# Kernel optimization log

Hardware: AMD Instinct MI355X
Metric: run time of the kernel (lower is better)

The kernel has to match this reference:

```python
import jax, jax.numpy as jnp
import numpy as np

B, S, H = 2, 2048, 2048
NH, NKV, D = 32, 8, 64
THETA = 10000.0
SCALE = 1.0 / float(np.sqrt(D))


def setup_inputs() -> dict:
    key = jax.random.key(0)
    k1, k2, k3 = jax.random.split(key, 3)
    return {
        "positions": jnp.arange(S, dtype=jnp.int32),
        "hidden_states": jax.random.normal(k1, (B, S, H), dtype=jnp.float32),
        "Wqkv": jax.random.normal(k2, (H, (NH + 2 * NKV) * D), dtype=jnp.float32) * 0.02,
        "Wo": jax.random.normal(k3, (NH * D, H), dtype=jnp.float32) * 0.02,
    }


def _rope_neox(x, cos, sin):
    # x: [B,S,h,D]; NeoX style: rotate_half over full rotary dim
    half = D // 2
    rot = jnp.concatenate([-x[..., half:], x[..., :half]], axis=-1)
    return x * cos + rot * sin


def reference(positions, hidden_states, Wqkv, Wo):
    # fused QKV projection
    qkv = jnp.einsum('bsh,hf->bsf', hidden_states, Wqkv)  # [B,S,(NH+2NKV)*D]
    q, k, v = jnp.split(qkv, [NH * D, NH * D + NKV * D], axis=-1)
    q = q.reshape(B, S, NH, D)
    k = k.reshape(B, S, NKV, D)
    v = v.reshape(B, S, NKV, D)

    # inline RoPE (full head_dim, NeoX style)
    inv_freq = 1.0 / (THETA ** (jnp.arange(0, D, 2, dtype=jnp.float32) / D))  # [D/2]
    freqs = positions.astype(jnp.float32)[:, None] * inv_freq  # [S,D/2]
    cos = jnp.concatenate([jnp.cos(freqs)] * 2, axis=-1)[None, :, None, :]  # [1,S,1,D]
    sin = jnp.concatenate([jnp.sin(freqs)] * 2, axis=-1)[None, :, None, :]
    q = _rope_neox(q, cos, sin)
    k = _rope_neox(k, cos, sin)

    # GQA: expand KV heads to match query heads
    g = NH // NKV
    k = jnp.repeat(k, g, axis=2)  # [B,S,NH,D]
    v = jnp.repeat(v, g, axis=2)

    # causal attention (prefill over the cached sequence)
    scores = jnp.einsum('bqhd,bkhd->bhqk', q, k) * SCALE  # [B,NH,S,S]
    causal = jnp.tril(jnp.ones((S, S), dtype=bool))
    scores = jnp.where(causal[None, None], scores, jnp.finfo(scores.dtype).min)
    attn = jax.nn.softmax(scores, axis=-1)
    ctx = jnp.einsum('bhqk,bkhd->bqhd', attn, v).reshape(B, S, NH * D)

    # output projection
    return jnp.einsum('bsf,fh->bsh', ctx, Wo)
```

## Files before the change

kernel.cpp:

```cpp
#include <hip/hip_runtime.h>
#include <hip/hip_bf16.h>
#include <math.h>

#define B_ 2
#define S_ 2048
#define H_ 2048
#define NH_ 32
#define NKV_ 8
#define D_ 64
#define F_ 3072
#define SCALE_ 0.125f
#define QSCALE_ 0.18033688011112042f
#define LN1E4_32_ 0.28782313662425575f

using bf16 = __bf16;
using bf16x4 = __attribute__((ext_vector_type(4))) __bf16;
using bf16x8 = __attribute__((ext_vector_type(8))) __bf16;
using f32x4 = __attribute__((ext_vector_type(4))) float;

#define GLOBAL_AS(p) ((__attribute__((address_space(1))) void*)(p))
#define LDS_AS(p)    ((__attribute__((address_space(3))) void*)(p))

__global__ void cvt_f32_bf16(const float4* __restrict__ in, bf16* __restrict__ out, int n4) {
    int i = blockIdx.x * 256 + threadIdx.x;
    if (i >= n4) return;
    float4 v = in[i];
    bf16x4 o = {(bf16)v.x, (bf16)v.y, (bf16)v.z, (bf16)v.w};
    *reinterpret_cast<bf16x4*>(out + (size_t)i * 4) = o;
}

__global__ void transpose_to_bf16(const float* __restrict__ in, bf16* __restrict__ out,
                                  int K, int N) {
    __shared__ float tile[32][33];
    int n0 = blockIdx.x * 32, k0 = blockIdx.y * 32;
    int tx = threadIdx.x, ty = threadIdx.y;
#pragma unroll
    for (int i = 0; i < 4; ++i)
        tile[ty + i * 8][tx] = in[(size_t)(k0 + ty + i * 8) * N + n0 + tx];
    __syncthreads();
#pragma unroll
    for (int i = 0; i < 4; ++i)
        out[(size_t)(n0 + ty + i * 8) * K + k0 + tx] = (bf16)tile[tx][ty + i * 8];
}

__global__ __launch_bounds__(256) void gemm_qkv_rope(const bf16* __restrict__ A,
                                                     const bf16* __restrict__ BT,
                                                     const int* __restrict__ positions,
                                                     bf16* __restrict__ Q,
                                                     bf16* __restrict__ Kb,
                                                     bf16* __restrict__ Vt) {
    __shared__ __attribute__((aligned(16))) bf16 As[128 * 32];
    __shared__ __attribute__((aligned(16))) bf16 Bs[128 * 32];
    const int tid = threadIdx.x;
    const int w = tid >> 6, lane = tid & 63;
    const int t = lane & 15, quad = lane >> 4;
    const int m0 = blockIdx.y * 128, n0 = blockIdx.x * 128;
    const int wm = (w >> 1) * 64, wn = (w & 1) * 64;
    const int lrow = lane >> 2;
    const int lcol = (lane & 3) * 8;

    f32x4 acc[4][4] = {};

    for (int k0 = 0; k0 < H_; k0 += 32) {
#pragma unroll
        for (int i = 0; i < 2; ++i) {
            int c = w * 2 + i;
            const bf16* ga = A + (size_t)(m0 + c * 16 + lrow) * H_ + k0 + lcol;
            __builtin_amdgcn_global_load_lds(GLOBAL_AS(ga), LDS_AS(As + c * 512), 16, 0, 0);
            const bf16* gb = BT + (size_t)(n0 + c * 16 + lrow) * H_ + k0 + lcol;
            __builtin_amdgcn_global_load_lds(GLOBAL_AS(gb), LDS_AS(Bs + c * 512), 16, 0, 0);
        }
        __syncthreads();
        bf16x8 a[4], b[4];
#pragma unroll
        for (int i = 0; i < 4; ++i)
            a[i] = *reinterpret_cast<const bf16x8*>(As + (wm + i * 16 + t) * 32 + quad * 8);
#pragma unroll
        for (int j = 0; j < 4; ++j)
            b[j] = *reinterpret_cast<const bf16x8*>(Bs + (wn + j * 16 + t) * 32 + quad * 8);
#pragma unroll
        for (int i = 0; i < 4; ++i)
#pragma unroll
            for (int j = 0; j < 4; ++j)
                acc[i][j] = __builtin_amdgcn_mfma_f32_16x16x32_bf16(a[i], b[j], acc[i][j], 0, 0, 0);
        __syncthreads();
    }

    const int hseg = (n0 + wn) >> 6;
    if (hseg < NH_ + NKV_) {
        const bool isQ = hseg < NH_;
        const float qs = isQ ? QSCALE_ : 1.0f;
        bf16* dst = isQ ? Q : Kb;
        const int hh = isQ ? hseg : hseg - NH_;
        const int nh = isQ ? NH_ : NKV_;
        const float inv0 = __expf(-(float)t * LN1E4_32_);
        const float inv1 = inv0 * 0.01f;
#pragma unroll
        for (int i = 0; i < 4; ++i)
#pragma unroll
            for (int r = 0; r < 4; ++r) {
                const int mrow = m0 + wm + i * 16 + quad * 4 + r;
                const int s = mrow & (S_ - 1), b = mrow >> 11;
                const float pos = (float)positions[s];
                float sn0, cs0, sn1, cs1;
                sincosf(pos * inv0, &sn0, &cs0);
                sincosf(pos * inv1, &sn1, &cs1);
                const float x0 = acc[i][0][r], x1 = acc[i][1][r];
                const float x2 = acc[i][2][r], x3 = acc[i][3][r];
                bf16 o0 = (bf16)((x0 * cs0 - x2 * sn0) * qs);
                bf16 o1 = (bf16)((x1 * cs1 - x3 * sn1) * qs);
                bf16 o2 = (bf16)((x2 * cs0 + x0 * sn0) * qs);
                bf16 o3 = (bf16)((x3 * cs1 + x1 * sn1) * qs);
                bf16* p = dst + ((size_t)(b * nh + hh) * S_ + s) * D_;
                p[t] = o0;
                p[16 + t] = o1;
                p[32 + t] = o2;
                p[48 + t] = o3;
            }
    } else {
        const int hv = hseg - NH_ - NKV_;
#pragma unroll
        for (int i = 0; i < 4; ++i)
#pragma unroll
            for (int r = 0; r < 4; ++r) {
                const int mrow = m0 + wm + i * 16 + quad * 4 + r;
                const int s = mrow & (S_ - 1), b = mrow >> 11;
                bf16* p = Vt + ((size_t)(b * NKV_ + hv) * D_) * S_ + s;
#pragma unroll
                for (int j = 0; j < 4; ++j)
                    p[(size_t)(j * 16 + t) * S_] = (bf16)acc[i][j][r];
            }
    }
}

__global__ __launch_bounds__(256) void gemm_bt(const bf16* __restrict__ A,
                                               const bf16* __restrict__ BT,
                                               float* __restrict__ C,
                                               int M, int N, int K) {
    __shared__ __attribute__((aligned(16))) bf16 As[128 * 32];
    __shared__ __attribute__((aligned(16))) bf16 Bs[128 * 32];
    const int tid = threadIdx.x;
    const int w = tid >> 6, lane = tid & 63;
    const int t = lane & 15, quad = lane >> 4;
    const int m0 = blockIdx.y * 128, n0 = blockIdx.x * 128;
    const int wm = (w >> 1) * 64, wn = (w & 1) * 64;
    const int lrow = lane >> 2;
    const int lcol = (lane & 3) * 8;

    f32x4 acc[4][4] = {};

    for (int k0 = 0; k0 < K; k0 += 32) {
#pragma unroll
        for (int i = 0; i < 2; ++i) {
            int c = w * 2 + i;
            const bf16* ga = A + (size_t)(m0 + c * 16 + lrow) * K + k0 + lcol;
            __builtin_amdgcn_global_load_lds(GLOBAL_AS(ga), LDS_AS(As + c * 512), 16, 0, 0);
            const bf16* gb = BT + (size_t)(n0 + c * 16 + lrow) * K + k0 + lcol;
            __builtin_amdgcn_global_load_lds(GLOBAL_AS(gb), LDS_AS(Bs + c * 512), 16, 0, 0);
        }
        __syncthreads();
        bf16x8 a[4], b[4];
#pragma unroll
        for (int i = 0; i < 4; ++i)
            a[i] = *reinterpret_cast<const bf16x8*>(As + (wm + i * 16 + t) * 32 + quad * 8);
#pragma unroll
        for (int j = 0; j < 4; ++j)
            b[j] = *reinterpret_cast<const bf16x8*>(Bs + (wn + j * 16 + t) * 32 + quad * 8);
#pragma unroll
        for (int i = 0; i < 4; ++i)
#pragma unroll
            for (int j = 0; j < 4; ++j)
                acc[i][j] = __builtin_amdgcn_mfma_f32_16x16x32_bf16(a[i], b[j], acc[i][j], 0, 0, 0);
        __syncthreads();
    }
#pragma unroll
    for (int i = 0; i < 4; ++i)
#pragma unroll
        for (int j = 0; j < 4; ++j)
#pragma unroll
            for (int r = 0; r < 4; ++r)
                C[(size_t)(m0 + wm + i * 16 + quad * 4 + r) * N + n0 + wn + j * 16 + t] =
                    acc[i][j][r];
}

__global__ __launch_bounds__(256, 4) void flash_attn(const bf16* __restrict__ Q,
                                                     const bf16* __restrict__ Kb,
                                                     const bf16* __restrict__ Vt,
                                                     bf16* __restrict__ ctx) {
    __shared__ __attribute__((aligned(16))) bf16 Ks[8 * 512];
    __shared__ __attribute__((aligned(16))) bf16 Vs[8 * 512];
    __shared__ __attribute__((aligned(16))) bf16 Plds[4][16 * 72];
    const int tid = threadIdx.x;
    const int w = tid >> 6, lane = tid & 63;
    const int t = lane & 15, quad = lane >> 4;
    const int kvh = blockIdx.y, b = blockIdx.z;
    const int h = kvh * 4 + w;
    const int bh = b * NH_ + h;
    const int bhk = b * NKV_ + kvh;
    const bf16* Kbase = Kb + (size_t)bhk * S_ * D_;
    const bf16* Vbase = Vt + (size_t)bhk * D_ * S_;

    for (int rep = 0; rep < 2; ++rep) {
        const int tileIdx = rep ? (127 - (int)blockIdx.x) : (int)blockIdx.x;
        const int qbase = tileIdx * 16;
        const int kend = qbase + 16;

        const bf16* Qp = Q + ((size_t)bh * S_ + qbase) * D_;
        bf16x8 qf0 = *reinterpret_cast<const bf16x8*>(Qp + t * D_ + quad * 8);
        bf16x8 qf1 = *reinterpret_cast<const bf16x8*>(Qp + t * D_ + 32 + quad * 8);

        f32x4 o[4] = {};
        float m = -1e30f, l = 0.f;

        for (int k0 = 0; k0 < kend; k0 += 64) {
            __syncthreads();
#pragma unroll
            for (int j = 0; j < 4; ++j) {
                const int c = w * 4 + j;
                if (c < 8) {
                    const int tl = c & 3, hf = c >> 2;
                    const bf16* src =
                        Kbase + (size_t)(k0 + tl * 16 + t) * D_ + hf * 32 + quad * 8;
                    __builtin_amdgcn_global_load_lds(GLOBAL_AS(src), LDS_AS(Ks + c * 512), 16, 0,
                                                     0);
                } else {
                    const int cv = c - 8, dt = cv & 3, hf = cv >> 2;
                    const bf16* src =
                        Vbase + (size_t)(dt * 16 + t) * S_ + k0 + hf * 32 + quad * 8;
                    __builtin_amdgcn_global_load_lds(GLOBAL_AS(src), LDS_AS(Vs + cv * 512), 16, 0,
                                                     0);
                }
            }
            __syncthreads();

            f32x4 sa[4] = {};
#pragma unroll
            for (int tl = 0; tl < 4; ++tl) {
                bf16x8 kf0 = *reinterpret_cast<const bf16x8*>(Ks + (tl)*512 + lane * 8);
                bf16x8 kf1 = *reinterpret_cast<const bf16x8*>(Ks + (4 + tl) * 512 + lane * 8);
                sa[tl] = __builtin_amdgcn_mfma_f32_16x16x32_bf16(kf0, qf0, sa[tl], 0, 0, 0);
                sa[tl] = __builtin_amdgcn_mfma_f32_16x16x32_bf16(kf1, qf1, sa[tl], 0, 0, 0);
            }
            if (k0 + 64 >= kend) {
                const int qrow = qbase + t;
#pragma unroll
                for (int tl = 0; tl < 4; ++tl)
#pragma unroll
                    for (int r = 0; r < 4; ++r)
                        if (k0 + tl * 16 + quad * 4 + r > qrow) sa[tl][r] = -1e30f;
            }
            float mx = -1e30f;
#pragma unroll
            for (int tl = 0; tl < 4; ++tl)
#pragma unroll
                for (int r = 0; r < 4; ++r) mx = fmaxf(mx, sa[tl][r]);
            mx = fmaxf(mx, __shfl_xor(mx, 16, 64));
            mx = fmaxf(mx, __shfl_xor(mx, 32, 64));
            const float mn = fmaxf(m, mx);
            const float alpha = exp2f(m - mn);
            m = mn;
            float rs = 0.f;
#pragma unroll
            for (int tl = 0; tl < 4; ++tl) {
                float p0 = exp2f(sa[tl][0] - mn);
                float p1 = exp2f(sa[tl][1] - mn);
                float p2 = exp2f(sa[tl][2] - mn);
                float p3 = exp2f(sa[tl][3] - mn);
                rs += (p0 + p1) + (p2 + p3);
                bf16x4 pk = {(bf16)p0, (bf16)p1, (bf16)p2, (bf16)p3};
                *reinterpret_cast<bf16x4*>(&Plds[w][t * 72 + tl * 16 + quad * 4]) = pk;
            }
#pragma unroll
            for (int dt = 0; dt < 4; ++dt)
#pragma unroll
                for (int r = 0; r < 4; ++r) o[dt][r] *= alpha;
            rs += __shfl_xor(rs, 16, 64);
            rs += __shfl_xor(rs, 32, 64);
            l = l * alpha + rs;

            asm volatile("s_waitcnt lgkmcnt(0)" ::: "memory");
            bf16x8 pf0 = *reinterpret_cast<const bf16x8*>(&Plds[w][t * 72 + quad * 8]);
            bf16x8 pf1 = *reinterpret_cast<const bf16x8*>(&Plds[w][t * 72 + 32 + quad * 8]);
            asm volatile("" ::: "memory");
#pragma unroll
            for (int dt = 0; dt < 4; ++dt) {
                bf16x8 vf0 = *reinterpret_cast<const bf16x8*>(Vs + (dt)*512 + lane * 8);
                bf16x8 vf1 = *reinterpret_cast<const bf16x8*>(Vs + (4 + dt) * 512 + lane * 8);
                o[dt] = __builtin_amdgcn_mfma_f32_16x16x32_bf16(vf0, pf0, o[dt], 0, 0, 0);
                o[dt] = __builtin_amdgcn_mfma_f32_16x16x32_bf16(vf1, pf1, o[dt], 0, 0, 0);
            }
        }
        const float inv = 1.0f / l;
        const size_t row = (size_t)b * S_ + qbase + t;
#pragma unroll
        for (int dt = 0; dt < 4; ++dt) {
            bf16x4 ov = {(bf16)(o[dt][0] * inv), (bf16)(o[dt][1] * inv),
                         (bf16)(o[dt][2] * inv), (bf16)(o[dt][3] * inv)};
            *reinterpret_cast<bf16x4*>(ctx + row * (NH_ * D_) + h * D_ + dt * 16 + quad * 4) = ov;
        }
    }
}

extern "C" void kernel_launch(void* const* d_in, const int* in_sizes, int n_in,
                              void* d_out, int out_size, void* d_ws, size_t ws_size,
                              hipStream_t stream) {
    const int* positions = (const int*)d_in[0];
    const float* hidden = (const float*)d_in[1];
    const float* Wqkv = (const float*)d_in[2];
    const float* Wo = (const float*)d_in[3];
    float* out = (float*)d_out;

    char* ws = (char*)d_ws;
    size_t off = 0;
    auto carve = [&](size_t bytes) {
        void* p = ws + off;
        off += (bytes + 255) & ~(size_t)255;
        return p;
    };
    bf16* hidB = (bf16*)carve((size_t)B_ * S_ * H_ * 2);
    bf16* WqkvT = (bf16*)carve((size_t)F_ * H_ * 2);
    bf16* WoT = (bf16*)carve((size_t)H_ * H_ * 2);
    bf16* Qb = (bf16*)carve((size_t)B_ * NH_ * S_ * D_ * 2);
    bf16* Kbb = (bf16*)carve((size_t)B_ * NKV_ * S_ * D_ * 2);
    bf16* Vt = (bf16*)carve((size_t)B_ * NKV_ * S_ * D_ * 2);
    bf16* ctx = (bf16*)carve((size_t)B_ * S_ * NH_ * D_ * 2);

    cvt_f32_bf16<<<(B_ * S_ * H_ / 4 + 255) / 256, 256, 0, stream>>>((const float4*)hidden, hidB,
                                                                     B_ * S_ * H_ / 4);
    transpose_to_bf16<<<dim3(F_ / 32, H_ / 32), dim3(32, 8), 0, stream>>>(Wqkv, WqkvT, H_, F_);
    transpose_to_bf16<<<dim3(H_ / 32, H_ / 32), dim3(32, 8), 0, stream>>>(Wo, WoT, H_, H_);
    gemm_qkv_rope<<<dim3(F_ / 128, (B_ * S_) / 128), 256, 0, stream>>>(hidB, WqkvT, positions, Qb,
                                                                       Kbb, Vt);
    flash_attn<<<dim3(64, NKV_, B_), 256, 0, stream>>>(Qb, Kbb, Vt, ctx);
    gemm_bt<<<dim3(H_ / 128, (B_ * S_) / 128), 256, 0, stream>>>(ctx, WoT, out, B_ * S_, H_, H_);
}
```

Before: 352.1 us.

## Double-buffer K/V tiles, share them across paired query tiles, swizzle P LDS

The flash attention kernel now processes both paired query tiles (i and 127-i) in one pass over the key range, so each K/V chunk loaded into LDS serves both tiles instead of being loaded twice. K/V staging is double-buffered: the next chunk is prefetched while the current one is processed, which also removes one barrier per iteration. The P scratch buffer drops its padding in favour of an XOR swizzle to avoid bank conflicts. In exchange, LDS use roughly doubles and register pressure rises from two sets of accumulators, which may lower occupancy under launch_bounds(256,4).

Result: faster. 335.7 us (-4.7%).

```diff
diff --git a/kernel.cpp b/kernel.cpp
--- a/kernel.cpp
+++ b/kernel.cpp
@@ -187,12 +187,13 @@
                                                      const bf16* __restrict__ Kb,
                                                      const bf16* __restrict__ Vt,
                                                      bf16* __restrict__ ctx) {
-    __shared__ __attribute__((aligned(16))) bf16 Ks[8 * 512];
-    __shared__ __attribute__((aligned(16))) bf16 Vs[8 * 512];
-    __shared__ __attribute__((aligned(16))) bf16 Plds[4][16 * 72];
+    __shared__ __attribute__((aligned(16))) bf16 Ks[2][8 * 512];
+    __shared__ __attribute__((aligned(16))) bf16 Vs[2][8 * 512];
+    __shared__ __attribute__((aligned(16))) bf16 Plds[4][16 * 64];
     const int tid = threadIdx.x;
     const int w = tid >> 6, lane = tid & 63;
     const int t = lane & 15, quad = lane >> 4;
+    const int sw = t & 7;
     const int kvh = blockIdx.y, b = blockIdx.z;
     const int h = kvh * 4 + w;
     const int bh = b * NH_ + h;
@@ -200,102 +201,129 @@
     const bf16* Kbase = Kb + (size_t)bhk * S_ * D_;
     const bf16* Vbase = Vt + (size_t)bhk * D_ * S_;
 
-    for (int rep = 0; rep < 2; ++rep) {
-        const int tileIdx = rep ? (127 - (int)blockIdx.x) : (int)blockIdx.x;
-        const int qbase = tileIdx * 16;
-        const int kend = qbase + 16;
-
-        const bf16* Qp = Q + ((size_t)bh * S_ + qbase) * D_;
-        bf16x8 qf0 = *reinterpret_cast<const bf16x8*>(Qp + t * D_ + quad * 8);
-        bf16x8 qf1 = *reinterpret_cast<const bf16x8*>(Qp + t * D_ + 32 + quad * 8);
-
-        f32x4 o[4] = {};
-        float m = -1e30f, l = 0.f;
-
-        for (int k0 = 0; k0 < kend; k0 += 64) {
-            __syncthreads();
-#pragma unroll
-            for (int j = 0; j < 4; ++j) {
-                const int c = w * 4 + j;
-                if (c < 8) {
-                    const int tl = c & 3, hf = c >> 2;
-                    const bf16* src =
-                        Kbase + (size_t)(k0 + tl * 16 + t) * D_ + hf * 32 + quad * 8;
-                    __builtin_amdgcn_global_load_lds(GLOBAL_AS(src), LDS_AS(Ks + c * 512), 16, 0,
-                                                     0);
-                } else {
-                    const int cv = c - 8, dt = cv & 3, hf = cv >> 2;
-                    const bf16* src =
-                        Vbase + (size_t)(dt * 16 + t) * S_ + k0 + hf * 32 + quad * 8;
-                    __builtin_amdgcn_global_load_lds(GLOBAL_AS(src), LDS_AS(Vs + cv * 512), 16, 0,
-                                                     0);
-                }
+    const int i = blockIdx.x;
+    const int qb0 = i * 16, qb1 = (127 - i) * 16;
+    const int kend0 = qb0 + 16, kend1 = qb1 + 16;
+
+    const bf16* Qp0 = Q + ((size_t)bh * S_ + qb0) * D_;
+    const bf16* Qp1 = Q + ((size_t)bh * S_ + qb1) * D_;
+    bf16x8 q0f0 = *reinterpret_cast<const bf16x8*>(Qp0 + t * D_ + quad * 8);
+    bf16x8 q0f1 = *reinterpret_cast<const bf16x8*>(Qp0 + t * D_ + 32 + quad * 8);
+    bf16x8 q1f0 = *reinterpret_cast<const bf16x8*>(Qp1 + t * D_ + quad * 8);
+    bf16x8 q1f1 = *reinterpret_cast<const bf16x8*>(Qp1 + t * D_ + 32 + quad * 8);
+
+    f32x4 o0[4] = {}, o1[4] = {};
+    float m0v = -1e30f, l0v = 0.f, m1v = -1e30f, l1v = 0.f;
+
+    auto stage = [&](int k0, int p) {
+#pragma unroll
+        for (int j = 0; j < 4; ++j) {
+            const int c = w * 4 + j;
+            if (c < 8) {
+                const int tl = c & 3, hf = c >> 2;
+                const bf16* src = Kbase + (size_t)(k0 + tl * 16 + t) * D_ + hf * 32 + quad * 8;
+                __builtin_amdgcn_global_load_lds(GLOBAL_AS(src), LDS_AS(&Ks[p][c * 512]), 16, 0,
+                                                 0);
+            } else {
+                const int cv = c - 8, dt = cv & 3, hf = cv >> 2;
+                const bf16* src = Vbase + (size_t)(dt * 16 + t) * S_ + k0 + hf * 32 + quad * 8;
+                __builtin_amdgcn_global_load_lds(GLOBAL_AS(src), LDS_AS(&Vs[p][cv * 512]), 16, 0,
+                                                 0);
             }
-            __syncthreads();
-
-            f32x4 sa[4] = {};
-#pragma unroll
-            for (int tl = 0; tl < 4; ++tl) {
-                bf16x8 kf0 = *reinterpret_cast<const bf16x8*>(Ks + (tl)*512 + lane * 8);
-                bf16x8 kf1 = *reinterpret_cast<const bf16x8*>(Ks + (4 + tl) * 512 + lane * 8);
-                sa[tl] = __builtin_amdgcn_mfma_f32_16x16x32_bf16(kf0, qf0, sa[tl], 0, 0, 0);
-                sa[tl] = __builtin_amdgcn_mfma_f32_16x16x32_bf16(kf1, qf1, sa[tl], 0, 0, 0);
-            }
-            if (k0 + 64 >= kend) {
-                const int qrow = qbase + t;
-#pragma unroll
-                for (int tl = 0; tl < 4; ++tl)
-#pragma unroll
-                    for (int r = 0; r < 4; ++r)
-                        if (k0 + tl * 16 + quad * 4 + r > qrow) sa[tl][r] = -1e30f;
-            }
-            float mx = -1e30f;
+        }
+    };
+
+    auto process = [&](const bf16* ks, const bf16* vs, bf16x8 qf0, bf16x8 qf1, float& m, float& l,
+                       f32x4* o, int k0, int qbase, bool domask) {
+        f32x4 sa[4] = {};
+#pragma unroll
+        for (int tl = 0; tl < 4; ++tl) {
+            bf16x8 kf0 = *reinterpret_cast<const bf16x8*>(ks + tl * 512 + lane * 8);
+            bf16x8 kf1 = *reinterpret_cast<const bf16x8*>(ks + (4 + tl) * 512 + lane * 8);
+            sa[tl] = __builtin_amdgcn_mfma_f32_16x16x32_bf16(kf0, qf0, sa[tl], 0, 0, 0);
+            sa[tl] = __builtin_amdgcn_mfma_f32_16x16x32_bf16(kf1, qf1, sa[tl], 0, 0, 0);
+        }
+        if (domask) {
+            const int qrow = qbase + t;
 #pragma unroll
             for (int tl = 0; tl < 4; ++tl)
 #pragma unroll
-                for (int r = 0; r < 4; ++r) mx = fmaxf(mx, sa[tl][r]);
-            mx = fmaxf(mx, __shfl_xor(mx, 16, 64));
-            mx = fmaxf(mx, __shfl_xor(mx, 32, 64));
-            const float mn = fmaxf(m, mx);
-            const float alpha = exp2f(m - mn);
-            m = mn;
-            float rs = 0.f;
-#pragma unroll
-            for (int tl = 0; tl < 4; ++tl) {
-                float p0 = exp2f(sa[tl][0] - mn);
-                float p1 = exp2f(sa[tl][1] - mn);
-                float p2 = exp2f(sa[tl][2] - mn);
-                float p3 = exp2f(sa[tl][3] - mn);
-                rs += (p0 + p1) + (p2 + p3);
-                bf16x4 pk = {(bf16)p0, (bf16)p1, (bf16)p2, (bf16)p3};
-                *reinterpret_cast<bf16x4*>(&Plds[w][t * 72 + tl * 16 + quad * 4]) = pk;
-            }
-#pragma unroll
-            for (int dt = 0; dt < 4; ++dt)
-#pragma unroll
-                for (int r = 0; r < 4; ++r) o[dt][r] *= alpha;
-            rs += __shfl_xor(rs, 16, 64);
-            rs += __shfl_xor(rs, 32, 64);
-            l = l * alpha + rs;
-
-            asm volatile("s_waitcnt lgkmcnt(0)" ::: "memory");
-            bf16x8 pf0 = *reinterpret_cast<const bf16x8*>(&Plds[w][t * 72 + quad * 8]);
-            bf16x8 pf1 = *reinterpret_cast<const bf16x8*>(&Plds[w][t * 72 + 32 + quad * 8]);
-            asm volatile("" ::: "memory");
-#pragma unroll
-            for (int dt = 0; dt < 4; ++dt) {
-                bf16x8 vf0 = *reinterpret_cast<const bf16x8*>(Vs + (dt)*512 + lane * 8);
-                bf16x8 vf1 = *reinterpret_cast<const bf16x8*>(Vs + (4 + dt) * 512 + lane * 8);
-                o[dt] = __builtin_amdgcn_mfma_f32_16x16x32_bf16(vf0, pf0, o[dt], 0, 0, 0);
-                o[dt] = __builtin_amdgcn_mfma_f32_16x16x32_bf16(vf1, pf1, o[dt], 0, 0, 0);
-            }
-        }
-        const float inv = 1.0f / l;
-        const size_t row = (size_t)b * S_ + qbase + t;
+                for (int r = 0; r < 4; ++r)
+                    if (k0 + tl * 16 + quad * 4 + r > qrow) sa[tl][r] = -1e30f;
+        }
+        float mx = -1e30f;
+#pragma unroll
+        for (int tl = 0; tl < 4; ++tl)
+#pragma unroll
+            for (int r = 0; r < 4; ++r) mx = fmaxf(mx, sa[tl][r]);
+        mx = fmaxf(mx, __shfl_xor(mx, 16, 64));
+        mx = fmaxf(mx, __shfl_xor(mx, 32, 64));
+        const float mn = fmaxf(m, mx);
+        const float alpha = exp2f(m - mn);
+        m = mn;
+        float rs = 0.f;
+#pragma unroll
+        for (int tl = 0; tl < 4; ++tl) {
+            float p0 = exp2f(sa[tl][0] - mn);
+            float p1 = exp2f(sa[tl][1] - mn);
+            float p2 = exp2f(sa[tl][2] - mn);
+            float p3 = exp2f(sa[tl][3] - mn);
+            rs += (p0 + p1) + (p2 + p3);
+            bf16x4 pk = {(bf16)p0, (bf16)p1, (bf16)p2, (bf16)p3};
+            *reinterpret_cast<bf16x4*>(
+                &Plds[w][t * 64 + (((tl * 2 + (quad >> 1)) ^ sw) << 3) + (quad & 1) * 4]) = pk;
+        }
+#pragma unroll
+        for (int dt = 0; dt < 4; ++dt)
+#pragma unroll
+            for (int r = 0; r < 4; ++r) o[dt][r] *= alpha;
+        rs += __shfl_xor(rs, 16, 64);
+        rs += __shfl_xor(rs, 32, 64);
+        l = l * alpha + rs;
+
+        asm volatile("s_waitcnt lgkmcnt(0)" ::: "memory");
+        bf16x8 pf0 = *reinterpret_cast<const bf16x8*>(&Plds[w][t * 64 + ((quad ^ sw) << 3)]);
+        bf16x8 pf1 =
+            *reinterpret_cast<const bf16x8*>(&Plds[w][t * 64 + (((4 + quad) ^ sw) << 3)]);
+        asm volatile("" ::: "memory");
 #pragma unroll
         for (int dt = 0; dt < 4; ++dt) {
-            bf16x4 ov = {(bf16)(o[dt][0] * inv), (bf16)(o[dt][1] * inv),
-                         (bf16)(o[dt][2] * inv), (bf16)(o[dt][3] * inv)};
+            bf16x8 vf0 = *reinterpret_cast<const bf16x8*>(vs + dt * 512 + lane * 8);
+            bf16x8 vf1 = *reinterpret_cast<const bf16x8*>(vs + (4 + dt) * 512 + lane * 8);
+            o[dt] = __builtin_amdgcn_mfma_f32_16x16x32_bf16(vf0, pf0, o[dt], 0, 0, 0);
+            o[dt] = __builtin_amdgcn_mfma_f32_16x16x32_bf16(vf1, pf1, o[dt], 0, 0, 0);
+        }
+    };
+
+    const int nch = (kend1 + 63) >> 6;
+    stage(0, 0);
+    for (int c = 0; c < nch; ++c) {
+        const int k0 = c << 6;
+        const int p = c & 1;
+        __syncthreads();
+        if (c + 1 < nch) stage((c + 1) << 6, p ^ 1);
+        process(&Ks[p][0], &Vs[p][0], q1f0, q1f1, m1v, l1v, o1, k0, qb1, k0 + 64 >= kend1);
+        if (k0 < kend0)
+            process(&Ks[p][0], &Vs[p][0], q0f0, q0f1, m0v, l0v, o0, k0, qb0, k0 + 64 >= kend0);
+    }
+
+    {
+        const float inv = 1.0f / l0v;
+        const size_t row = (size_t)b * S_ + qb0 + t;
+#pragma unroll
+        for (int dt = 0; dt < 4; ++dt) {
+            bf16x4 ov = {(bf16)(o0[dt][0] * inv), (bf16)(o0[dt][1] * inv),
+                         (bf16)(o0[dt][2] * inv), (bf16)(o0[dt][3] * inv)};
+            *reinterpret_cast<bf16x4*>(ctx + row * (NH_ * D_) + h * D_ + dt * 16 + quad * 4) = ov;
+        }
+    }
+    {
+        const float inv = 1.0f / l1v;
+        const size_t row = (size_t)b * S_ + qb1 + t;
+#pragma unroll
+        for (int dt = 0; dt < 4; ++dt) {
+            bf16x4 ov = {(bf16)(o1[dt][0] * inv), (bf16)(o1[dt][1] * inv),
+                         (bf16)(o1[dt][2] * inv), (bf16)(o1[dt][3] * inv)};
             *reinterpret_cast<bf16x4*>(ctx + row * (NH_ * D_) + h * D_ + dt * 16 + quad * 4) = ov;
         }
     }
```
